# Kernel tuning notes

Measured on AMD Instinct MI355X. Metric: run time of the kernel, lower is better.

The kernel has to match this reference:

```python
import jax, jax.numpy as jnp
import numpy as np

DIM = 768
DIM_QKV = 64
NUM_HEAD = 12
EPS = 1e-5


def layer_norm(x, gamma, beta):
    mu = jnp.mean(x, axis=-1, keepdims=True)
    var = jnp.mean(jnp.square(x - mu), axis=-1, keepdims=True)
    return (x - mu) * jax.lax.rsqrt(var + EPS) * gamma + beta


def setup_inputs() -> dict:
    key = jax.random.key(0)
    ks = jax.random.split(key, 10)
    s = 0.02
    x = jax.random.normal(ks[0], (4, 2048, DIM), dtype=jnp.float32)
    wq = jax.random.normal(ks[1], (DIM, DIM_QKV), dtype=jnp.float32) * s
    wk = jax.random.normal(ks[2], (DIM, DIM_QKV), dtype=jnp.float32) * s
    wv = jax.random.normal(ks[3], (DIM, DIM_QKV), dtype=jnp.float32) * s
    lin_w = jax.random.normal(ks[4], (DIM_QKV * NUM_HEAD, DIM), dtype=jnp.float32) * s
    lin_b = jnp.zeros((DIM,), dtype=jnp.float32)
    ln1_g = jnp.ones((DIM,), dtype=jnp.float32)
    ln1_b = jnp.zeros((DIM,), dtype=jnp.float32)
    fc1_w = jax.random.normal(ks[5], (DIM, 4 * DIM), dtype=jnp.float32) * s
    fc1_b = jnp.zeros((4 * DIM,), dtype=jnp.float32)
    fc2_w = jax.random.normal(ks[6], (4 * DIM, DIM), dtype=jnp.float32) * s
    fc2_b = jnp.zeros((DIM,), dtype=jnp.float32)
    return {"x": x, "wq": wq, "wk": wk, "wv": wv, "lin_w": lin_w,
            "lin_b": lin_b, "ln1_g": ln1_g, "ln1_b": ln1_b,
            "fc1_w": fc1_w, "fc1_b": fc1_b, "fc2_w": fc2_w, "fc2_b": fc2_b}


def reference(x, wq, wk, wv, lin_w, lin_b, ln1_g, ln1_b, fc1_w, fc1_b, fc2_w, fc2_b):
    identity1 = x
    h = layer_norm(x, ln1_g, ln1_b)
    # single shared-weight attention head (original calls the same module num_head times)
    q = h @ wq  # [B,S,Dq]
    k = h @ wk
    v = h @ wv
    scores = jnp.einsum('bik,bjk->bij', q, k) / (DIM_QKV ** 0.5)  # [B,S,S]
    attn = jax.nn.softmax(scores, axis=-1)
    out_head = attn @ v  # [B,S,Dq]
    # concat of num_head identical outputs == tile along last dim
    cat = jnp.tile(out_head, (1, 1, NUM_HEAD))  # [B,S,Dq*H]
    attn_out = cat @ lin_w + lin_b
    out = attn_out + identity1
    identity2 = out
    # NOTE: original reuses layer_norm_1 here (layer_norm_2 is unused)
    out = layer_norm(out, ln1_g, ln1_b)
    out = jax.nn.gelu(out @ fc1_w + fc1_b, approximate=False)
    out = out @ fc2_w + fc2_b
    return out + identity2
```

## Files before the change

### kernel.cpp

```cpp
#include <hip/hip_runtime.h>

typedef unsigned short u16;
typedef unsigned int u32;
typedef __bf16 bf16x8 __attribute__((ext_vector_type(8)));
typedef float f32x4 __attribute__((ext_vector_type(4)));

__device__ __forceinline__ u16 f2bf(float f) {
  u32 u = __float_as_uint(f);
  u32 r = (u + 0x7FFFu + ((u >> 16) & 1u)) >> 16;
  return (u16)r;
}

__device__ __forceinline__ float gelu_exact(float x) {
  return 0.5f * x * (1.f + erff(x * 0.70710678118654752f));
}

__device__ __forceinline__ void gload16(const u16* g, u16* l) {
  __builtin_amdgcn_global_load_lds((const __attribute__((address_space(1))) void*)g,
                                   (__attribute__((address_space(3))) void*)l, 16, 0, 0);
}

__global__ void transpose_cast(const float* __restrict__ in, u16* __restrict__ out,
                               int R, int C) {
  __shared__ float tile[32][33];
  int c0 = blockIdx.x * 32, r0 = blockIdx.y * 32;
  int tx = threadIdx.x, ty = threadIdx.y;
  for (int i = 0; i < 32; i += 8) {
    int r = r0 + ty + i, c = c0 + tx;
    tile[ty + i][tx] = (r < R && c < C) ? in[(long)r * C + c] : 0.f;
  }
  __syncthreads();
  for (int i = 0; i < 32; i += 8) {
    int oc = c0 + ty + i, orr = r0 + tx;
    if (oc < C && orr < R) out[(long)oc * R + orr] = f2bf(tile[tx][ty + i]);
  }
}

__global__ void weff_build(const float* __restrict__ lin_w, u16* __restrict__ weffT) {
  int idx = blockIdx.x * 256 + threadIdx.x;
  if (idx >= 768 * 64) return;
  int n = idx % 768, d = idx / 768;
  float s = 0.f;
#pragma unroll
  for (int j = 0; j < 12; j++) s += lin_w[(long)(j * 64 + d) * 768 + n];
  weffT[(long)n * 64 + d] = f2bf(s);
}

__global__ __launch_bounds__(256)
void ln_rows(const float* __restrict__ in, const float* __restrict__ gamma,
             const float* __restrict__ beta, u16* __restrict__ out, int nrows) {
  int gid = blockIdx.x * blockDim.x + threadIdx.x;
  int wid = gid >> 6, l = gid & 63;
  if (wid >= nrows) return;
  const float4* row = (const float4*)(in + (long)wid * 768);
  float4 v[3];
  float s = 0.f, s2 = 0.f;
#pragma unroll
  for (int j = 0; j < 3; j++) {
    v[j] = row[l + 64 * j];
    s += v[j].x + v[j].y + v[j].z + v[j].w;
    s2 += v[j].x * v[j].x + v[j].y * v[j].y + v[j].z * v[j].z + v[j].w * v[j].w;
  }
#pragma unroll
  for (int off = 1; off < 64; off <<= 1) {
    s += __shfl_xor(s, off);
    s2 += __shfl_xor(s2, off);
  }
  float mean = s * (1.f / 768.f);
  float rstd = rsqrtf(s2 * (1.f / 768.f) - mean * mean + 1e-5f);
  u16* orow = out + (long)wid * 768;
#pragma unroll
  for (int j = 0; j < 3; j++) {
    float4 g = ((const float4*)gamma)[l + 64 * j];
    float4 b = ((const float4*)beta)[l + 64 * j];
    ushort4 o;
    o.x = f2bf((v[j].x - mean) * rstd * g.x + b.x);
    o.y = f2bf((v[j].y - mean) * rstd * g.y + b.y);
    o.z = f2bf((v[j].z - mean) * rstd * g.z + b.z);
    o.w = f2bf((v[j].w - mean) * rstd * g.w + b.w);
    ((ushort4*)orow)[l + 64 * j] = o;
  }
}

template <int EPI>
__global__ __launch_bounds__(256, 2)
void gemm_bt(const u16* __restrict__ A, const u16* __restrict__ Bt,
             const float* __restrict__ bias, const float* __restrict__ res,
             void* __restrict__ outv, int M, int N, int K, int ldo) {
  __shared__ __align__(16) u16 Alds[2][128 * 32];
  __shared__ __align__(16) u16 Blds[2][128 * 32];
  const int t = threadIdx.x;
  const int w = t >> 6, l = t & 63;
  const int wr = w >> 1, wc = w & 1;
  const int srow = w * 32 + (l >> 2);
  const int scol = (l & 3) * 8;
  const u16* aptr = A + (long)(blockIdx.x * 128 + srow) * K + scol;
  const u16* bptr = Bt + (long)(blockIdx.y * 128 + srow) * K + scol;
  const long j16 = (long)16 * K;
  const int lw = (w * 32) * 32;
  const int ar = (wr * 64 + (l & 15)) * 32 + (l >> 4) * 8;
  const int br = (wc * 64 + (l & 15)) * 32 + (l >> 4) * 8;
  f32x4 acc[4][4] = {};
  const int ksteps = K >> 5;
  gload16(aptr, &Alds[0][lw]);
  gload16(aptr + j16, &Alds[0][lw + 16 * 32]);
  gload16(bptr, &Blds[0][lw]);
  gload16(bptr + j16, &Blds[0][lw + 16 * 32]);
  aptr += 32;
  bptr += 32;
  __syncthreads();
  for (int ks = 0; ks < ksteps; ks++) {
    const int cur = ks & 1;
    if (ks + 1 < ksteps) {
      const int nxt = cur ^ 1;
      gload16(aptr, &Alds[nxt][lw]);
      gload16(aptr + j16, &Alds[nxt][lw + 16 * 32]);
      gload16(bptr, &Blds[nxt][lw]);
      gload16(bptr + j16, &Blds[nxt][lw + 16 * 32]);
      aptr += 32;
      bptr += 32;
    }
    bf16x8 af[4], bfr[4];
#pragma unroll
    for (int i = 0; i < 4; i++) af[i] = *(const bf16x8*)(&Alds[cur][ar + i * 16 * 32]);
#pragma unroll
    for (int i = 0; i < 4; i++) bfr[i] = *(const bf16x8*)(&Blds[cur][br + i * 16 * 32]);
#pragma unroll
    for (int mf = 0; mf < 4; mf++)
#pragma unroll
      for (int nf = 0; nf < 4; nf++)
        acc[mf][nf] = __builtin_amdgcn_mfma_f32_16x16x32_bf16(af[mf], bfr[nf], acc[mf][nf], 0, 0, 0);
    __syncthreads();
  }
  const int rowbase = blockIdx.x * 128 + wr * 64 + ((l >> 4) * 4);
  const int colbase = blockIdx.y * 128 + wc * 64 + (l & 15);
#pragma unroll
  for (int nf = 0; nf < 4; nf++) {
    int col = colbase + nf * 16;
    if (col >= N) continue;
    float bv = (EPI == 0) ? 0.f : bias[col];
#pragma unroll
    for (int mf = 0; mf < 4; mf++) {
#pragma unroll
      for (int i = 0; i < 4; i++) {
        long row = rowbase + mf * 16 + i;
        float v = acc[mf][nf][i] + bv;
        if (EPI == 2) v = gelu_exact(v);
        if (EPI == 1) {
          v += res[row * ldo + col];
          ((float*)outv)[row * ldo + col] = v;
        } else {
          ((u16*)outv)[row * ldo + col] = f2bf(v);
        }
      }
    }
  }
}

__global__ __launch_bounds__(128)
void attn_fwd(const u16* __restrict__ qkv, float* __restrict__ pout,
              float* __restrict__ pm, float* __restrict__ pl) {
  __shared__ __align__(16) u16 Klds[32 * 72];
  __shared__ __align__(16) u16 Vlds[64 * 40];
  __shared__ __align__(16) u16 Plds[2][16 * 40];
  const int t = threadIdx.x, w = t >> 6, l = t & 63;
  const int r0 = blockIdx.x * 32;
  const int sp = blockIdx.y;
  const long bb = (long)(r0 & ~2047);
  const int qrow = r0 + w * 16 + (l & 15);
  bf16x8 qf0 = *(const bf16x8*)(qkv + (long)qrow * 192 + ((l >> 4) * 8));
  bf16x8 qf1 = *(const bf16x8*)(qkv + (long)qrow * 192 + 32 + ((l >> 4) * 8));
  f32x4 po[4] = {};
  float m_i[4], l_i[4];
#pragma unroll
  for (int i = 0; i < 4; i++) { m_i[i] = -1e30f; l_i[i] = 0.f; }
  const int kkey = t >> 3, kseg = t & 7;
  for (int st = sp * 256; st < sp * 256 + 256; st += 32) {
    uint4 k0 = *(const uint4*)(qkv + (bb + st + kkey) * 192 + 64 + kseg * 8);
    uint4 k1 = *(const uint4*)(qkv + (bb + st + 16 + kkey) * 192 + 64 + kseg * 8);
    u16 vv[16];
#pragma unroll
    for (int i = 0; i < 16; i++) {
      int e = t + 128 * i;
      vv[i] = qkv[(bb + st + (e >> 6)) * 192 + 128 + (e & 63)];
    }
    __syncthreads();
    *(uint4*)(&Klds[kkey * 72 + kseg * 8]) = k0;
    *(uint4*)(&Klds[(16 + kkey) * 72 + kseg * 8]) = k1;
#pragma unroll
    for (int i = 0; i < 16; i++) {
      int e = t + 128 * i;
      Vlds[(e & 63) * 40 + (e >> 6)] = vv[i];
    }
    __syncthreads();
    f32x4 s0 = {}, s1 = {};
    {
      bf16x8 ka = *(const bf16x8*)(&Klds[(l & 15) * 72 + ((l >> 4) * 8)]);
      bf16x8 kb = *(const bf16x8*)(&Klds[(l & 15) * 72 + 32 + ((l >> 4) * 8)]);
      s0 = __builtin_amdgcn_mfma_f32_16x16x32_bf16(qf0, ka, s0, 0, 0, 0);
      s0 = __builtin_amdgcn_mfma_f32_16x16x32_bf16(qf1, kb, s0, 0, 0, 0);
      bf16x8 kc = *(const bf16x8*)(&Klds[(16 + (l & 15)) * 72 + ((l >> 4) * 8)]);
      bf16x8 kd = *(const bf16x8*)(&Klds[(16 + (l & 15)) * 72 + 32 + ((l >> 4) * 8)]);
      s1 = __builtin_amdgcn_mfma_f32_16x16x32_bf16(qf0, kc, s1, 0, 0, 0);
      s1 = __builtin_amdgcn_mfma_f32_16x16x32_bf16(qf1, kd, s1, 0, 0, 0);
    }
    float sf[4];
#pragma unroll
    for (int i = 0; i < 4; i++) {
      float a = s0[i] * 0.125f, b = s1[i] * 0.125f;
      float tm = fmaxf(a, b);
#pragma unroll
      for (int off = 1; off < 16; off <<= 1) tm = fmaxf(tm, __shfl_xor(tm, off));
      float mn = fmaxf(m_i[i], tm);
      sf[i] = __expf(m_i[i] - mn);
      m_i[i] = mn;
      a = __expf(a - mn);
      b = __expf(b - mn);
      float rs = a + b;
#pragma unroll
      for (int off = 1; off < 16; off <<= 1) rs += __shfl_xor(rs, off);
      l_i[i] = l_i[i] * sf[i] + rs;
      int prow = (l >> 4) * 4 + i;
      Plds[w][prow * 40 + (l & 15)] = f2bf(a);
      Plds[w][prow * 40 + 16 + (l & 15)] = f2bf(b);
    }
#pragma unroll
    for (int n = 0; n < 4; n++)
#pragma unroll
      for (int i = 0; i < 4; i++) po[n][i] *= sf[i];
    bf16x8 pf = *(const bf16x8*)(&Plds[w][(l & 15) * 40 + ((l >> 4) * 8)]);
#pragma unroll
    for (int n = 0; n < 4; n++) {
      bf16x8 vf = *(const bf16x8*)(&Vlds[(n * 16 + (l & 15)) * 40 + ((l >> 4) * 8)]);
      po[n] = __builtin_amdgcn_mfma_f32_16x16x32_bf16(pf, vf, po[n], 0, 0, 0);
    }
  }
#pragma unroll
  for (int i = 0; i < 4; i++) {
    long row = r0 + w * 16 + ((l >> 4) * 4) + i;
    if ((l & 15) == 0) {
      pm[(long)sp * 8192 + row] = m_i[i];
      pl[(long)sp * 8192 + row] = l_i[i];
    }
#pragma unroll
    for (int n = 0; n < 4; n++)
      pout[((long)sp * 8192 + row) * 64 + n * 16 + (l & 15)] = po[n][i];
  }
}

__global__ __launch_bounds__(256)
void attn_merge(const float* __restrict__ pout, const float* __restrict__ pm,
                const float* __restrict__ pl, u16* __restrict__ oh) {
  int gid = blockIdx.x * 256 + threadIdx.x;
  int row = gid >> 6;
  float M = -1e30f;
#pragma unroll
  for (int s = 0; s < 8; s++) M = fmaxf(M, pm[s * 8192 + row]);
  float L = 0.f, acc = 0.f;
#pragma unroll
  for (int s = 0; s < 8; s++) {
    float e = __expf(pm[s * 8192 + row] - M);
    L += pl[s * 8192 + row] * e;
    acc += pout[((long)s * 8192 + row) * 64 + (gid & 63)] * e;
  }
  oh[gid] = f2bf(acc / L);
}

extern "C" void kernel_launch(void* const* d_in, const int* in_sizes, int n_in,
                              void* d_out, int out_size, void* d_ws, size_t ws_size,
                              hipStream_t stream) {
  const float* x = (const float*)d_in[0];
  const float* wq = (const float*)d_in[1];
  const float* wk = (const float*)d_in[2];
  const float* wv = (const float*)d_in[3];
  const float* lin_w = (const float*)d_in[4];
  const float* lin_b = (const float*)d_in[5];
  const float* ln1_g = (const float*)d_in[6];
  const float* ln1_b = (const float*)d_in[7];
  const float* fc1_w = (const float*)d_in[8];
  const float* fc1_b = (const float*)d_in[9];
  const float* fc2_w = (const float*)d_in[10];
  const float* fc2_b = (const float*)d_in[11];
  float* out = (float*)d_out;

  char* p = (char*)d_ws;
  u16* wqkvT = (u16*)p; p += 256 * 768 * 2;
  u16* weffT = (u16*)p; p += 768 * 64 * 2;
  u16* fc1wT = (u16*)p; p += (size_t)3072 * 768 * 2;
  u16* fc2wT = (u16*)p; p += (size_t)768 * 3072 * 2;
  u16* h = (u16*)p; p += (size_t)8192 * 768 * 2;
  u16* qkv = (u16*)p; p += (size_t)8192 * 192 * 2;
  u16* oh = (u16*)p; p += (size_t)8192 * 64 * 2;
  float* out1 = (float*)p; p += (size_t)8192 * 768 * 4;
  u16* a1 = (u16*)p; p += (size_t)8192 * 3072 * 2;
  float* pout = (float*)a1;
  float* pm = pout + (size_t)8 * 8192 * 64;
  float* pl = pm + 8 * 8192;

  dim3 tb(32, 8);
  transpose_cast<<<dim3(2, 24), tb, 0, stream>>>(wq, wqkvT, 768, 64);
  transpose_cast<<<dim3(2, 24), tb, 0, stream>>>(wk, wqkvT + 64 * 768, 768, 64);
  transpose_cast<<<dim3(2, 24), tb, 0, stream>>>(wv, wqkvT + 128 * 768, 768, 64);
  hipMemsetAsync(wqkvT + 192 * 768, 0, 64 * 768 * 2, stream);
  transpose_cast<<<dim3(96, 24), tb, 0, stream>>>(fc1_w, fc1wT, 768, 3072);
  transpose_cast<<<dim3(24, 96), tb, 0, stream>>>(fc2_w, fc2wT, 3072, 768);
  weff_build<<<192, 256, 0, stream>>>(lin_w, weffT);

  ln_rows<<<2048, 256, 0, stream>>>(x, ln1_g, ln1_b, h, 8192);
  gemm_bt<0><<<dim3(64, 2), 256, 0, stream>>>(h, wqkvT, nullptr, nullptr, qkv,
                                              8192, 192, 768, 192);
  attn_fwd<<<dim3(256, 8), 128, 0, stream>>>(qkv, pout, pm, pl);
  attn_merge<<<2048, 256, 0, stream>>>(pout, pm, pl, oh);
  gemm_bt<1><<<dim3(64, 6), 256, 0, stream>>>(oh, weffT, lin_b, x, out1,
                                              8192, 768, 64, 768);
  ln_rows<<<2048, 256, 0, stream>>>(out1, ln1_g, ln1_b, h, 8192);
  gemm_bt<2><<<dim3(64, 24), 256, 0, stream>>>(h, fc1wT, fc1_b, nullptr, a1,
                                               8192, 3072, 768, 3072);
  gemm_bt<1><<<dim3(64, 6), 256, 0, stream>>>(a1, fc2wT, fc2_b, out1, out,
                                              8192, 768, 3072, 768);
}
```

Measured before the change: 339.9 us.

## Triple-buffer GEMM LDS pipeline with XOR swizzle and explicit waitcnt barriers

Moves the bf16 GEMM's LDS staging from two buffers to three, so global-to-LDS loads run two k-steps ahead. Explicit vmcnt waits and raw s_barrier calls replace __syncthreads, so only the oldest outstanding stage must land before a barrier. It also XOR-swizzles the 16-byte column chunks on both the load-to-LDS and fragment-read sides to cut LDS bank conflicts. Launch bounds are raised to ask for three blocks per CU. The costs are 1.5x LDS per block, which may limit occupancy, and hand-counted vmcnt values that are fragile.

Measured after the change: 338.7 us. No clear change (-0.4%).

```diff
diff --git a/kernel.cpp b/kernel.cpp
--- a/kernel.cpp
+++ b/kernel.cpp
@@ -83,54 +83,62 @@
 }
 
 template <int EPI>
-__global__ __launch_bounds__(256, 2)
+__global__ __launch_bounds__(256, 3)
 void gemm_bt(const u16* __restrict__ A, const u16* __restrict__ Bt,
              const float* __restrict__ bias, const float* __restrict__ res,
              void* __restrict__ outv, int M, int N, int K, int ldo) {
-  __shared__ __align__(16) u16 Alds[2][128 * 32];
-  __shared__ __align__(16) u16 Blds[2][128 * 32];
+  __shared__ __align__(16) u16 Alds[3][128 * 32];
+  __shared__ __align__(16) u16 Blds[3][128 * 32];
   const int t = threadIdx.x;
   const int w = t >> 6, l = t & 63;
   const int wr = w >> 1, wc = w & 1;
   const int srow = w * 32 + (l >> 2);
-  const int scol = (l & 3) * 8;
+  const int scol = ((l & 3) ^ ((l >> 3) & 3)) * 8;
   const u16* aptr = A + (long)(blockIdx.x * 128 + srow) * K + scol;
   const u16* bptr = Bt + (long)(blockIdx.y * 128 + srow) * K + scol;
   const long j16 = (long)16 * K;
   const int lw = (w * 32) * 32;
-  const int ar = (wr * 64 + (l & 15)) * 32 + (l >> 4) * 8;
-  const int br = (wc * 64 + (l & 15)) * 32 + (l >> 4) * 8;
+  const int key = ((l & 15) >> 1) & 3;
+  const int ar = (wr * 64 + (l & 15)) * 32 + (((l >> 4) ^ key) * 8);
+  const int br = (wc * 64 + (l & 15)) * 32 + (((l >> 4) ^ key) * 8);
   f32x4 acc[4][4] = {};
   const int ksteps = K >> 5;
-  gload16(aptr, &Alds[0][lw]);
-  gload16(aptr + j16, &Alds[0][lw + 16 * 32]);
-  gload16(bptr, &Blds[0][lw]);
-  gload16(bptr + j16, &Blds[0][lw + 16 * 32]);
-  aptr += 32;
-  bptr += 32;
-  __syncthreads();
+
+  auto STAGE = [&](int s, int buf) {
+    const u16* ap = aptr + (long)s * 32;
+    const u16* bp = bptr + (long)s * 32;
+    gload16(ap, &Alds[buf][lw]);
+    gload16(ap + j16, &Alds[buf][lw + 16 * 32]);
+    gload16(bp, &Blds[buf][lw]);
+    gload16(bp + j16, &Blds[buf][lw + 16 * 32]);
+  };
+
+  STAGE(0, 0);
+  STAGE(1, 1);
+  asm volatile("s_waitcnt vmcnt(4)" ::: "memory");
+  __builtin_amdgcn_s_barrier();
   for (int ks = 0; ks < ksteps; ks++) {
-    const int cur = ks & 1;
-    if (ks + 1 < ksteps) {
-      const int nxt = cur ^ 1;
-      gload16(aptr, &Alds[nxt][lw]);
-      gload16(aptr + j16, &Alds[nxt][lw + 16 * 32]);
-      gload16(bptr, &Blds[nxt][lw]);
-      gload16(bptr + j16, &Blds[nxt][lw + 16 * 32]);
-      aptr += 32;
-      bptr += 32;
-    }
+    const int cur = ks % 3;
+    if (ks + 2 < ksteps) STAGE(ks + 2, (ks + 2) % 3);
     bf16x8 af[4], bfr[4];
 #pragma unroll
     for (int i = 0; i < 4; i++) af[i] = *(const bf16x8*)(&Alds[cur][ar + i * 16 * 32]);
 #pragma unroll
     for (int i = 0; i < 4; i++) bfr[i] = *(const bf16x8*)(&Blds[cur][br + i * 16 * 32]);
+    asm volatile("s_waitcnt lgkmcnt(0)" ::: "memory");
+    __builtin_amdgcn_sched_barrier(0);
 #pragma unroll
     for (int mf = 0; mf < 4; mf++)
 #pragma unroll
       for (int nf = 0; nf < 4; nf++)
         acc[mf][nf] = __builtin_amdgcn_mfma_f32_16x16x32_bf16(af[mf], bfr[nf], acc[mf][nf], 0, 0, 0);
-    __syncthreads();
+    if (ks < ksteps - 2) {
+      asm volatile("s_waitcnt vmcnt(4)" ::: "memory");
+      __builtin_amdgcn_s_barrier();
+    } else if (ks == ksteps - 2) {
+      asm volatile("s_waitcnt vmcnt(0)" ::: "memory");
+      __builtin_amdgcn_s_barrier();
+    }
   }
   const int rowbase = blockIdx.x * 128 + wr * 64 + ((l >> 4) * 4);
   const int colbase = blockIdx.y * 128 + wc * 64 + (l & 15);
```
